# Performance work log

Hardware: AMD Instinct MI355X
Metric: run time of the kernel (lower is better)

## Reference

```python
import jax, jax.numpy as jnp
import numpy as np

B, T, D, H = 4, 2048, 1024, 16
DK = D // H  # 64


def setup_inputs() -> dict:
    key = jax.random.key(0)
    ks = jax.random.split(key, 8)
    std = 1.0 / np.sqrt(2.0 * D)  # initialize_weights: normal(0, 1/sqrt(2*d_model*(i_layer+1))), i_layer=0
    inp = {
        "q": jax.random.normal(ks[0], (B, T, D), jnp.float32),
        "k": jax.random.normal(ks[1], (B, T, D), jnp.float32),
        "v": jax.random.normal(ks[2], (B, T, D), jnp.float32),
        "Wq": jax.random.normal(ks[3], (D, D), jnp.float32) * std,
        "Wk": jax.random.normal(ks[4], (D, D), jnp.float32) * std,
        "Wv": jax.random.normal(ks[5], (D, D), jnp.float32) * std,
        "Wo": jax.random.normal(ks[6], (D, D), jnp.float32) * std,
        "bq": jnp.zeros((D,), jnp.float32),
        "bk": jnp.zeros((D,), jnp.float32),
        "bv": jnp.zeros((D,), jnp.float32),
        "bo": jnp.zeros((D,), jnp.float32),
    }
    return inp


def _split_heads(x):
    # (B,T,D) -> (B,H,T,DK), same as x.view(B,T,H,DK).transpose(1,2)
    b, t, _ = x.shape
    return x.reshape(b, t, H, DK).transpose(0, 2, 1, 3)


def reference(q, k, v, Wq, Wk, Wv, Wo, bq, bk, bv, bo):
    # Linear projections (torch Linear: x @ W.T + b)
    qh = _split_heads(q @ Wq.T + bq)  # (B,H,T,DK)
    kh = _split_heads(k @ Wk.T + bk)
    vh = _split_heads(v @ Wv.T + bv)

    # scaled dot-product similarities: (B,H,Tq,Tk)
    scores = jnp.einsum("bhqd,bhkd->bhqk", qh, kh) / jnp.sqrt(jnp.float32(DK))

    # causal mask: tril(ones)==0 positions filled with -inf
    tq, tk = scores.shape[-2], scores.shape[-1]
    causal = jnp.tril(jnp.ones((tq, tk), dtype=bool))
    scores = jnp.where(causal, scores, jnp.float32(-jnp.inf))

    attn = jax.nn.softmax(scores, axis=-1)  # (B,H,Tq,Tk)
    ctx = jnp.einsum("bhqk,bhkd->bhqd", attn, vh)  # (B,H,Tq,DK)

    # merge heads: (B,H,T,DK) -> (B,T,D), then output projection
    merged = ctx.transpose(0, 2, 1, 3).reshape(q.shape[0], tq, D)
    return merged @ Wo.T + bo
```

## Files before the change

### kernel.cpp

```cpp
#include <hip/hip_runtime.h>
#include <hip/hip_bf16.h>
#include <stdint.h>

#define B_ 4
#define T_ 2048
#define D_ 1024
#define H_ 16
#define DK_ 64
#define M_ (B_*T_)

typedef __attribute__((ext_vector_type(8))) short bf16x8;
typedef __attribute__((ext_vector_type(4))) short bf16x4;
typedef __attribute__((ext_vector_type(4))) float f32x4;
typedef __hip_bfloat16 bf16;

__device__ __forceinline__ void gld_lds16(const bf16* g, bf16* l) {
  __builtin_amdgcn_global_load_lds((const __attribute__((address_space(1))) void*)g,
                                   (__attribute__((address_space(3))) void*)l,
                                   16, 0, 0);
}
__device__ __forceinline__ void gld_lds16f(const float* g, float* l) {
  __builtin_amdgcn_global_load_lds((const __attribute__((address_space(1))) void*)g,
                                   (__attribute__((address_space(3))) void*)l,
                                   16, 0, 0);
}

__device__ __forceinline__ short bfbits(float f) {
  union { bf16 h; short s; } u; u.h = __float2bfloat16(f); return u.s;
}

__global__ __launch_bounds__(256) void cvt_w(
    const float* __restrict__ wq, const float* __restrict__ wk,
    const float* __restrict__ wv, const float* __restrict__ wo,
    bf16* __restrict__ wqb, bf16* __restrict__ wkb,
    bf16* __restrict__ wvb, bf16* __restrict__ wob) {
  int gid = blockIdx.x * 256 + threadIdx.x;
  int s = gid >> 18, off = gid & 262143;
  const float* src = (s == 0) ? wq : (s == 1) ? wk : (s == 2) ? wv : wo;
  bf16* dst = (s == 0) ? wqb : (s == 1) ? wkb : (s == 2) ? wvb : wob;
  float4 val = reinterpret_cast<const float4*>(src)[off];
  union { ushort4 u; bf16 h[4]; } o;
  o.h[0] = __float2bfloat16(val.x);
  o.h[1] = __float2bfloat16(val.y);
  o.h[2] = __float2bfloat16(val.z);
  o.h[3] = __float2bfloat16(val.w);
  reinterpret_cast<ushort4*>(dst)[off] = o.u;
}

__global__ __launch_bounds__(512) void proj_qkv(
    const float* __restrict__ qf, const float* __restrict__ kf, const float* __restrict__ vf,
    const bf16* __restrict__ Wqb, const bf16* __restrict__ Wkb, const bf16* __restrict__ Wvb,
    const float* __restrict__ bq, const float* __restrict__ bk, const float* __restrict__ bv,
    bf16* __restrict__ Qh, bf16* __restrict__ Kh, bf16* __restrict__ Vt) {
  constexpr int K = 1024;
  constexpr int BK = 64;
  __shared__ __align__(16) bf16  As[256 * 64];
  __shared__ __align__(16) float Bsf[128 * 64];

  const int z = blockIdx.z;
  const bf16*  A  = (z == 0) ? Wqb : (z == 1) ? Wkb : Wvb;
  const float* Bf = (z == 0) ? qf : (z == 1) ? kf : vf;
  const float* bias = (z == 0) ? bq : (z == 1) ? bk : bv;
  bf16* out = (z == 0) ? Qh : (z == 1) ? Kh : Vt;
  const float scale = (z == 0) ? 0.125f * 1.4426950408889634f : 1.0f;

  const int bid = blockIdx.x + 32 * blockIdx.y;
  const int bm = bid >> 6;
  const int bn = bid & 63;

  const int tid = threadIdx.x;
  const int w = tid >> 6, l = tid & 63;
  const int wm = w >> 1, wn = w & 1;
  const int lr = l & 15, lk = l >> 4;

  f32x4 acc[4][4] = {};

  for (int k0 = 0; k0 < K; k0 += BK) {
#pragma unroll
    for (int i = 0; i < 4; ++i) {
      int p = i * 512 + tid;
      int row = p >> 3;
      int so = (p & 7) ^ (row & 7);
      gld_lds16(A + (size_t)(bm * 256 + row) * K + k0 + so * 8, &As[p * 8]);
    }
#pragma unroll
    for (int i = 0; i < 4; ++i) {
      int p = i * 512 + tid;
      int row = p >> 4;
      int sc = (p & 15) ^ (row & 15);
      gld_lds16f(Bf + (size_t)(bn * 128 + row) * K + k0 + sc * 4, &Bsf[p * 4]);
    }
    __syncthreads();

#pragma unroll
    for (int kk = 0; kk < 2; ++kk) {
      bf16x8 af[4], bfr[4];
#pragma unroll
      for (int m = 0; m < 4; ++m) {
        int row = wm * 64 + m * 16 + lr;
        int slot = (kk * 4 + lk) ^ (row & 7);
        af[m] = *reinterpret_cast<const bf16x8*>(&As[row * 64 + slot * 8]);
      }
#pragma unroll
      for (int n = 0; n < 4; ++n) {
        int trow = wn * 64 + n * 16 + lr;
        int c0 = kk * 8 + lk * 2;
        int s0 = c0 ^ (trow & 15);
        int s1 = (c0 + 1) ^ (trow & 15);
        f32x4 lo = *reinterpret_cast<const f32x4*>(&Bsf[trow * 64 + s0 * 4]);
        f32x4 hi = *reinterpret_cast<const f32x4*>(&Bsf[trow * 64 + s1 * 4]);
        bf16x8 bb;
        bb[0] = bfbits(lo[0]); bb[1] = bfbits(lo[1]);
        bb[2] = bfbits(lo[2]); bb[3] = bfbits(lo[3]);
        bb[4] = bfbits(hi[0]); bb[5] = bfbits(hi[1]);
        bb[6] = bfbits(hi[2]); bb[7] = bfbits(hi[3]);
        bfr[n] = bb;
      }
      __builtin_amdgcn_s_setprio(1);
#pragma unroll
      for (int m = 0; m < 4; ++m)
#pragma unroll
        for (int n = 0; n < 4; ++n)
          acc[m][n] = __builtin_amdgcn_mfma_f32_16x16x32_bf16(af[m], bfr[n], acc[m][n], 0, 0, 0);
      __builtin_amdgcn_s_setprio(0);
    }
    __syncthreads();
  }

  const int crow0 = bm * 256 + wm * 64;
  const int ccol0 = bn * 128 + wn * 64;
  if (z < 2) {
#pragma unroll
    for (int m = 0; m < 4; ++m) {
#pragma unroll
      for (int n = 0; n < 4; ++n) {
        const int row0 = crow0 + m * 16 + lk * 4;
        const int col = ccol0 + n * 16 + lr;
        bf16x4 pk;
#pragma unroll
        for (int r = 0; r < 4; ++r)
          pk[r] = bfbits((acc[m][n][r] + bias[row0 + r]) * scale);
        size_t idx = (((size_t)(col >> 11) * H_ + (row0 >> 6)) * T_ + (col & (T_ - 1))) * DK_ + (row0 & 63);
        *reinterpret_cast<bf16x4*>(&out[idx]) = pk;
      }
    }
  } else {
#pragma unroll
    for (int m = 0; m < 4; ++m) {
#pragma unroll
      for (int n = 0; n < 4; ++n) {
#pragma unroll
        for (int r = 0; r < 4; ++r) {
          const int row = crow0 + m * 16 + lk * 4 + r;
          const int col = ccol0 + n * 16 + lr;
          float vv = acc[m][n][r] + bias[row];
          size_t idx = (size_t)(col >> 11) * ((size_t)H_ * DK_ * T_) + (size_t)row * T_ + (col & (T_ - 1));
          out[idx] = __float2bfloat16(vv);
        }
      }
    }
  }
}

__global__ __launch_bounds__(512) void gemm_out(const bf16* __restrict__ A,
                                                const bf16* __restrict__ Bm,
                                                const float* __restrict__ bias,
                                                float* __restrict__ Cout) {
  constexpr int K = 1024;
  constexpr int BK = 64;
  __shared__ __align__(16) bf16 As[256 * BK];
  __shared__ __align__(16) bf16 Bs[128 * BK];

  const int bid = blockIdx.x + 32 * blockIdx.y;
  const int xcd = bid & 7, loc = bid >> 3;
  const int bm = xcd * 4 + (loc & 3);
  const int bn = loc >> 2;

  const int tid = threadIdx.x;
  const int w = tid >> 6, l = tid & 63;
  const int wm = w >> 1, wn = w & 1;
  const int lr = l & 15, lk = l >> 4;

  f32x4 acc[4][4] = {};

  for (int k0 = 0; k0 < K; k0 += BK) {
#pragma unroll
    for (int i = 0; i < 4; ++i) {
      int p = i * 512 + tid;
      int row = p >> 3;
      int so = (p & 7) ^ (row & 7);
      gld_lds16(A + (size_t)(bm * 256 + row) * K + k0 + so * 8, &As[p * 8]);
    }
#pragma unroll
    for (int i = 0; i < 2; ++i) {
      int p = i * 512 + tid;
      int row = p >> 3;
      int so = (p & 7) ^ (row & 7);
      gld_lds16(Bm + (size_t)(bn * 128 + row) * K + k0 + so * 8, &Bs[p * 8]);
    }
    __syncthreads();

#pragma unroll
    for (int kk = 0; kk < 2; ++kk) {
      bf16x8 af[4], bfr[4];
#pragma unroll
      for (int m = 0; m < 4; ++m) {
        int row = wm * 64 + m * 16 + lr;
        int slot = (kk * 4 + lk) ^ (row & 7);
        af[m] = *reinterpret_cast<const bf16x8*>(&As[row * BK + slot * 8]);
      }
#pragma unroll
      for (int n = 0; n < 4; ++n) {
        int row = wn * 64 + n * 16 + lr;
        int slot = (kk * 4 + lk) ^ (row & 7);
        bfr[n] = *reinterpret_cast<const bf16x8*>(&Bs[row * BK + slot * 8]);
      }
#pragma unroll
      for (int m = 0; m < 4; ++m)
#pragma unroll
        for (int n = 0; n < 4; ++n)
          acc[m][n] = __builtin_amdgcn_mfma_f32_16x16x32_bf16(af[m], bfr[n], acc[m][n], 0, 0, 0);
    }
    __syncthreads();
  }

  const int crow0 = bm * 256 + wm * 64;
  const int ccol0 = bn * 128 + wn * 64;
#pragma unroll
  for (int m = 0; m < 4; ++m) {
#pragma unroll
    for (int n = 0; n < 4; ++n) {
#pragma unroll
      for (int r = 0; r < 4; ++r) {
        const int row = crow0 + m * 16 + lk * 4 + r;
        const int col = ccol0 + n * 16 + lr;
        Cout[(size_t)row * D_ + col] = acc[m][n][r] + bias[col];
      }
    }
  }
}

__global__ __launch_bounds__(256, 7) void attn_fwd(const bf16* __restrict__ Qh,
                                                   const bf16* __restrict__ Kh,
                                                   const bf16* __restrict__ Vt,
                                                   bf16* __restrict__ ctx) {
  __shared__ __align__(16) bf16 Kbuf[2][32 * 64];
  __shared__ __align__(16) bf16 Vbuf[2][32 * 64];
  __shared__ __align__(16) char Ps[4][16 * 80];

  const int tid = threadIdx.x, w = tid >> 6, l = tid & 63;
  const int lr = l & 15, lk = l >> 4;
  const int bid = blockIdx.x;
  const int head = bid & 63;
  const int t = 31 - (bid >> 6);
  char* Pw = &Ps[w][0];

  const bf16* Qb = Qh + (size_t)head * T_ * DK_;
  const bf16* Kb = Kh + (size_t)head * T_ * DK_;
  const bf16* Vb = Vt + (size_t)head * DK_ * T_;
  const int bb = head >> 4, hh = head & 15;

  const int r0 = t * 64;
  const int nt32 = 2 * (t + 1);
  const int qrow = r0 + w * 16 + lr;
  const int jd = (r0 + w * 16) >> 5;

  const bf16* qp = Qb + (size_t)qrow * DK_ + lk * 8;
  bf16x8 qf0 = *reinterpret_cast<const bf16x8*>(qp);
  bf16x8 qf1 = *reinterpret_cast<const bf16x8*>(qp + 32);

  const int p = tid;
  const int krow = p >> 3, kso = (p & 7) ^ (krow & 7);
  const bf16* kgp = Kb + (size_t)krow * DK_ + kso * 8;
  const int vu = (p & 7) ^ (krow & 7);
  const int vdk = krow * 2 + (vu >> 2);
  const bf16* vgp = Vb + (size_t)vdk * T_ + (vu & 3) * 8;
  bf16* const kl0 = &Kbuf[0][p * 8];
  bf16* const kl1 = &Kbuf[1][p * 8];
  bf16* const vl0 = &Vbuf[0][p * 8];
  bf16* const vl1 = &Vbuf[1][p * 8];

  int qko[2][2], pwo[2], pvo[4];
#pragma unroll
  for (int n = 0; n < 2; ++n) {
    const int row = n * 16 + lr;
    qko[n][0] = row * 64 + ((lk ^ (row & 7)) << 3);
    qko[n][1] = row * 64 + (((4 + lk) ^ (row & 7)) << 3);
    pwo[n] = lr * 80 + n * 32 + lk * 8;
  }
  const int pro = lr * 80 + lk * 16;
#pragma unroll
  for (int n = 0; n < 4; ++n) {
    const int rowp = n * 8 + (lr >> 1);
    const int s = ((lr & 1) * 4 + lk) ^ (rowp & 7);
    pvo[n] = rowp * 64 + s * 8;
  }
  bf16* const cp = &ctx[((size_t)(bb * T_ + qrow)) * D_ + hh * DK_ + lk * 4];

  f32x4 oacc[4] = {};
  float srow = 0.f;

  gld_lds16(kgp, kl0);
  gld_lds16(vgp, vl0);
  kgp += 32 * DK_;
  vgp += 32;
  __syncthreads();

  int buf = 0;
#pragma unroll 1
  for (int j = 0; j < nt32; ++j) {
    if (j + 1 < nt32) {
      gld_lds16(kgp, buf ? kl0 : kl1);
      gld_lds16(vgp, buf ? vl0 : vl1);
      kgp += 32 * DK_;
      vgp += 32;
    }

    if (j <= jd) {
      const bf16* kbase = buf ? &Kbuf[1][0] : &Kbuf[0][0];
      const bf16* vbase = buf ? &Vbuf[1][0] : &Vbuf[0][0];

      f32x4 sacc[2] = {};
      __builtin_amdgcn_s_setprio(1);
#pragma unroll
      for (int n = 0; n < 2; ++n) {
        bf16x8 kf0 = *reinterpret_cast<const bf16x8*>(kbase + qko[n][0]);
        bf16x8 kf1 = *reinterpret_cast<const bf16x8*>(kbase + qko[n][1]);
        sacc[n] = __builtin_amdgcn_mfma_f32_16x16x32_bf16(kf0, qf0, sacc[n], 0, 0, 0);
        sacc[n] = __builtin_amdgcn_mfma_f32_16x16x32_bf16(kf1, qf1, sacc[n], 0, 0, 0);
      }
      __builtin_amdgcn_s_setprio(0);

      if (j == jd) {
#pragma unroll
        for (int n = 0; n < 2; ++n)
#pragma unroll
          for (int r = 0; r < 4; ++r)
            if (j * 32 + n * 16 + lk * 4 + r > qrow) sacc[n][r] = -1e30f;
      }

      float ts = 0.f;
#pragma unroll
      for (int n = 0; n < 2; ++n) {
        float p0 = __builtin_exp2f(sacc[n][0]);
        float p1 = __builtin_exp2f(sacc[n][1]);
        float p2 = __builtin_exp2f(sacc[n][2]);
        float p3 = __builtin_exp2f(sacc[n][3]);
        ts += (p0 + p1) + (p2 + p3);
        bf16x4 pk;
        pk[0] = bfbits(p0); pk[1] = bfbits(p1); pk[2] = bfbits(p2); pk[3] = bfbits(p3);
        *reinterpret_cast<bf16x4*>(Pw + pwo[n]) = pk;
      }
      ts += __shfl_xor(ts, 16, 64);
      ts += __shfl_xor(ts, 32, 64);
      srow += ts;

      bf16x8 pa = *reinterpret_cast<const bf16x8*>(Pw + pro);

      __builtin_amdgcn_s_setprio(1);
#pragma unroll
      for (int n = 0; n < 4; ++n) {
        bf16x8 vf = *reinterpret_cast<const bf16x8*>(vbase + pvo[n]);
        oacc[n] = __builtin_amdgcn_mfma_f32_16x16x32_bf16(vf, pa, oacc[n], 0, 0, 0);
      }
      __builtin_amdgcn_s_setprio(0);
    }

    __syncthreads();
    buf ^= 1;
  }

  const float inv = 1.0f / srow;
#pragma unroll
  for (int n = 0; n < 4; ++n) {
    bf16x4 pk;
#pragma unroll
    for (int r = 0; r < 4; ++r) pk[r] = bfbits(oacc[n][r] * inv);
    *reinterpret_cast<bf16x4*>(cp + n * 16) = pk;
  }
}

extern "C" void kernel_launch(void* const* d_in, const int* in_sizes, int n_in,
                              void* d_out, int out_size, void* d_ws, size_t ws_size,
                              hipStream_t stream) {
  const float* q  = (const float*)d_in[0];
  const float* k  = (const float*)d_in[1];
  const float* v  = (const float*)d_in[2];
  const float* Wq = (const float*)d_in[3];
  const float* Wk = (const float*)d_in[4];
  const float* Wv = (const float*)d_in[5];
  const float* Wo = (const float*)d_in[6];
  const float* bq = (const float*)d_in[7];
  const float* bk = (const float*)d_in[8];
  const float* bv = (const float*)d_in[9];
  const float* bo = (const float*)d_in[10];

  constexpr size_t E_IN = (size_t)M_ * D_;
  constexpr size_t E_W  = (size_t)D_ * D_;
  char* ws = (char*)d_ws;
  size_t off = 0;
  bf16* Wqb = (bf16*)(ws + off); off += E_W * 2;
  bf16* Wkb = (bf16*)(ws + off); off += E_W * 2;
  bf16* Wvb = (bf16*)(ws + off); off += E_W * 2;
  bf16* Wob = (bf16*)(ws + off); off += E_W * 2;
  bf16* Qh  = (bf16*)(ws + off); off += E_IN * 2;
  bf16* Kh  = (bf16*)(ws + off); off += E_IN * 2;
  bf16* Vtw = (bf16*)(ws + off); off += E_IN * 2;
  bf16* ctx = (bf16*)(ws + off); off += E_IN * 2;

  cvt_w<<<dim3(4096), dim3(256), 0, stream>>>(Wq, Wk, Wv, Wo, Wqb, Wkb, Wvb, Wob);

  proj_qkv<<<dim3(32, 8, 3), dim3(512), 0, stream>>>(q, k, v, Wqb, Wkb, Wvb,
                                                     bq, bk, bv, Qh, Kh, Vtw);

  attn_fwd<<<dim3(2048), dim3(256), 0, stream>>>(Qh, Kh, Vtw, ctx);

  gemm_out<<<dim3(32, 8), dim3(512), 0, stream>>>(ctx, Wob, bo, (float*)d_out);
}
```

Before: 188.6 us.

## Process two 16-row query groups per wave to double K/V tile reuse

Each attention block now covers 128 query rows instead of 64, with every wave handling two 16-row query groups that share the same K and V fragments loaded from LDS. This halves the grid, halves the global K/V traffic per query row and amortizes LDS reads and barriers over twice the MFMA work. In exchange it uses more registers (launch bound lowered from 7 to 6 blocks), needs a second P scratch buffer per wave, and leaves fewer, larger blocks, which can hurt load balance across the triangular causal workload.

Result: slower. 336.9 us (+78.6%).

```diff
diff --git a/kernel.cpp b/kernel.cpp
--- a/kernel.cpp
+++ b/kernel.cpp
@@ -240,34 +240,36 @@
   }
 }
 
-__global__ __launch_bounds__(256, 7) void attn_fwd(const bf16* __restrict__ Qh,
+__global__ __launch_bounds__(256, 6) void attn_fwd(const bf16* __restrict__ Qh,
                                                    const bf16* __restrict__ Kh,
                                                    const bf16* __restrict__ Vt,
                                                    bf16* __restrict__ ctx) {
   __shared__ __align__(16) bf16 Kbuf[2][32 * 64];
   __shared__ __align__(16) bf16 Vbuf[2][32 * 64];
-  __shared__ __align__(16) char Ps[4][16 * 80];
+  __shared__ __align__(16) char Ps[4][2][16 * 80];
 
   const int tid = threadIdx.x, w = tid >> 6, l = tid & 63;
   const int lr = l & 15, lk = l >> 4;
   const int bid = blockIdx.x;
   const int head = bid & 63;
-  const int t = 31 - (bid >> 6);
-  char* Pw = &Ps[w][0];
+  const int t = 15 - (bid >> 6);
 
   const bf16* Qb = Qh + (size_t)head * T_ * DK_;
   const bf16* Kb = Kh + (size_t)head * T_ * DK_;
   const bf16* Vb = Vt + (size_t)head * DK_ * T_;
   const int bb = head >> 4, hh = head & 15;
 
-  const int r0 = t * 64;
-  const int nt32 = 2 * (t + 1);
-  const int qrow = r0 + w * 16 + lr;
-  const int jd = (r0 + w * 16) >> 5;
-
-  const bf16* qp = Qb + (size_t)qrow * DK_ + lk * 8;
-  bf16x8 qf0 = *reinterpret_cast<const bf16x8*>(qp);
-  bf16x8 qf1 = *reinterpret_cast<const bf16x8*>(qp + 32);
+  const int base = t * 128 + w * 32;
+  const int nt32 = 4 * (t + 1);
+  const int jd = base >> 5;
+
+  bf16x8 qf[2][2];
+#pragma unroll
+  for (int g = 0; g < 2; ++g) {
+    const bf16* qp = Qb + (size_t)(base + g * 16 + lr) * DK_ + lk * 8;
+    qf[g][0] = *reinterpret_cast<const bf16x8*>(qp);
+    qf[g][1] = *reinterpret_cast<const bf16x8*>(qp + 32);
+  }
 
   const int p = tid;
   const int krow = p >> 3, kso = (p & 7) ^ (krow & 7);
@@ -280,25 +282,25 @@
   bf16* const vl0 = &Vbuf[0][p * 8];
   bf16* const vl1 = &Vbuf[1][p * 8];
 
-  int qko[2][2], pwo[2], pvo[4];
+  int qko[2][2], pvo[4];
 #pragma unroll
   for (int n = 0; n < 2; ++n) {
     const int row = n * 16 + lr;
     qko[n][0] = row * 64 + ((lk ^ (row & 7)) << 3);
     qko[n][1] = row * 64 + (((4 + lk) ^ (row & 7)) << 3);
-    pwo[n] = lr * 80 + n * 32 + lk * 8;
-  }
-  const int pro = lr * 80 + lk * 16;
+  }
 #pragma unroll
   for (int n = 0; n < 4; ++n) {
     const int rowp = n * 8 + (lr >> 1);
     const int s = ((lr & 1) * 4 + lk) ^ (rowp & 7);
     pvo[n] = rowp * 64 + s * 8;
   }
-  bf16* const cp = &ctx[((size_t)(bb * T_ + qrow)) * D_ + hh * DK_ + lk * 4];
-
-  f32x4 oacc[4] = {};
-  float srow = 0.f;
+  char* const Pw0 = &Ps[w][0][0];
+  char* const Pw1 = &Ps[w][1][0];
+  const int pro = lr * 80 + lk * 16;
+
+  f32x4 oacc[2][4] = {};
+  float srow[2] = { 0.f, 0.f };
 
   gld_lds16(kgp, kl0);
   gld_lds16(vgp, vl0);
@@ -320,48 +322,59 @@
       const bf16* kbase = buf ? &Kbuf[1][0] : &Kbuf[0][0];
       const bf16* vbase = buf ? &Vbuf[1][0] : &Vbuf[0][0];
 
-      f32x4 sacc[2] = {};
+      f32x4 sacc[2][2] = {};
       __builtin_amdgcn_s_setprio(1);
 #pragma unroll
       for (int n = 0; n < 2; ++n) {
         bf16x8 kf0 = *reinterpret_cast<const bf16x8*>(kbase + qko[n][0]);
         bf16x8 kf1 = *reinterpret_cast<const bf16x8*>(kbase + qko[n][1]);
-        sacc[n] = __builtin_amdgcn_mfma_f32_16x16x32_bf16(kf0, qf0, sacc[n], 0, 0, 0);
-        sacc[n] = __builtin_amdgcn_mfma_f32_16x16x32_bf16(kf1, qf1, sacc[n], 0, 0, 0);
+        sacc[0][n] = __builtin_amdgcn_mfma_f32_16x16x32_bf16(kf0, qf[0][0], sacc[0][n], 0, 0, 0);
+        sacc[0][n] = __builtin_amdgcn_mfma_f32_16x16x32_bf16(kf1, qf[0][1], sacc[0][n], 0, 0, 0);
+        sacc[1][n] = __builtin_amdgcn_mfma_f32_16x16x32_bf16(kf0, qf[1][0], sacc[1][n], 0, 0, 0);
+        sacc[1][n] = __builtin_amdgcn_mfma_f32_16x16x32_bf16(kf1, qf[1][1], sacc[1][n], 0, 0, 0);
       }
       __builtin_amdgcn_s_setprio(0);
 
       if (j == jd) {
 #pragma unroll
-        for (int n = 0; n < 2; ++n)
-#pragma unroll
-          for (int r = 0; r < 4; ++r)
-            if (j * 32 + n * 16 + lk * 4 + r > qrow) sacc[n][r] = -1e30f;
-      }
-
-      float ts = 0.f;
-#pragma unroll
-      for (int n = 0; n < 2; ++n) {
-        float p0 = __builtin_exp2f(sacc[n][0]);
-        float p1 = __builtin_exp2f(sacc[n][1]);
-        float p2 = __builtin_exp2f(sacc[n][2]);
-        float p3 = __builtin_exp2f(sacc[n][3]);
-        ts += (p0 + p1) + (p2 + p3);
-        bf16x4 pk;
-        pk[0] = bfbits(p0); pk[1] = bfbits(p1); pk[2] = bfbits(p2); pk[3] = bfbits(p3);
-        *reinterpret_cast<bf16x4*>(Pw + pwo[n]) = pk;
-      }
-      ts += __shfl_xor(ts, 16, 64);
-      ts += __shfl_xor(ts, 32, 64);
-      srow += ts;
-
-      bf16x8 pa = *reinterpret_cast<const bf16x8*>(Pw + pro);
+        for (int g = 0; g < 2; ++g) {
+          const int qrow = base + g * 16 + lr;
+#pragma unroll
+          for (int n = 0; n < 2; ++n)
+#pragma unroll
+            for (int r = 0; r < 4; ++r)
+              if (j * 32 + n * 16 + lk * 4 + r > qrow) sacc[g][n][r] = -1e30f;
+        }
+      }
+
+      bf16x8 pa[2];
+#pragma unroll
+      for (int g = 0; g < 2; ++g) {
+        char* Pw = g ? Pw1 : Pw0;
+        float ts = 0.f;
+#pragma unroll
+        for (int n = 0; n < 2; ++n) {
+          float p0 = __builtin_exp2f(sacc[g][n][0]);
+          float p1 = __builtin_exp2f(sacc[g][n][1]);
+          float p2 = __builtin_exp2f(sacc[g][n][2]);
+          float p3 = __builtin_exp2f(sacc[g][n][3]);
+          ts += (p0 + p1) + (p2 + p3);
+          bf16x4 pk;
+          pk[0] = bfbits(p0); pk[1] = bfbits(p1); pk[2] = bfbits(p2); pk[3] = bfbits(p3);
+          *reinterpret_cast<bf16x4*>(Pw + lr * 80 + n * 32 + lk * 8) = pk;
+        }
+        ts += __shfl_xor(ts, 16, 64);
+        ts += __shfl_xor(ts, 32, 64);
+        srow[g] += ts;
+        pa[g] = *reinterpret_cast<const bf16x8*>(Pw + pro);
+      }
 
       __builtin_amdgcn_s_setprio(1);
 #pragma unroll
       for (int n = 0; n < 4; ++n) {
         bf16x8 vf = *reinterpret_cast<const bf16x8*>(vbase + pvo[n]);
-        oacc[n] = __builtin_amdgcn_mfma_f32_16x16x32_bf16(vf, pa, oacc[n], 0, 0, 0);
+        oacc[0][n] = __builtin_amdgcn_mfma_f32_16x16x32_bf16(vf, pa[0], oacc[0][n], 0, 0, 0);
+        oacc[1][n] = __builtin_amdgcn_mfma_f32_16x16x32_bf16(vf, pa[1], oacc[1][n], 0, 0, 0);
       }
       __builtin_amdgcn_s_setprio(0);
     }
@@ -370,13 +383,17 @@
     buf ^= 1;
   }
 
-  const float inv = 1.0f / srow;
-#pragma unroll
-  for (int n = 0; n < 4; ++n) {
-    bf16x4 pk;
-#pragma unroll
-    for (int r = 0; r < 4; ++r) pk[r] = bfbits(oacc[n][r] * inv);
-    *reinterpret_cast<bf16x4*>(cp + n * 16) = pk;
+#pragma unroll
+  for (int g = 0; g < 2; ++g) {
+    const float inv = 1.0f / srow[g];
+    bf16* cp = &ctx[((size_t)(bb * T_ + base + g * 16 + lr)) * D_ + hh * DK_ + lk * 4];
+#pragma unroll
+    for (int n = 0; n < 4; ++n) {
+      bf16x4 pk;
+#pragma unroll
+      for (int r = 0; r < 4; ++r) pk[r] = bfbits(oacc[g][n][r] * inv);
+      *reinterpret_cast<bf16x4*>(cp + n * 16) = pk;
+    }
   }
 }
 
@@ -413,7 +430,7 @@
   proj_qkv<<<dim3(32, 8, 3), dim3(512), 0, stream>>>(q, k, v, Wqb, Wkb, Wvb,
                                                      bq, bk, bv, Qh, Kh, Vtw);
 
-  attn_fwd<<<dim3(2048), dim3(256), 0, stream>>>(Qh, Kh, Vtw, ctx);
+  attn_fwd<<<dim3(1024), dim3(256), 0, stream>>>(Qh, Kh, Vtw, ctx);
 
   gemm_out<<<dim3(32, 8), dim3(512), 0, stream>>>(ctx, Wob, bo, (float*)d_out);
 }
```
